# Kernel optimization log

Measured on AMD Instinct MI355X. Metric: run time of the kernel, lower is better.

Reference implementation:

```python
import jax, jax.numpy as jnp
import numpy as np

B, L, D, H, DH, FF = 4, 1024, 1024, 16, 64, 4096
EPS = 1e-5


def _layer_norm(x, g, b):
    m = jnp.mean(x, -1, keepdims=True)
    v = jnp.mean((x - m) ** 2, -1, keepdims=True)
    return (x - m) * jax.lax.rsqrt(v + EPS) * g + b


def setup_inputs() -> dict:
    key = jax.random.key(0)
    ks = jax.random.split(key, 20)
    s = 0.02  # param init scale
    return {
        "x": jax.random.normal(ks[0], (B, L, D), jnp.float32),
        "adj_mask_matrix": jax.random.uniform(ks[1], (B * H, L, L), jnp.float32),
        "com_mask_matrix": jax.random.uniform(ks[2], (B * H, L, L), jnp.float32),
        "lattice_rel": jax.random.normal(ks[3], (2, 1, 1, DH), jnp.float32),
        "Wq": jax.random.normal(ks[4], (D, D), jnp.float32) * s,
        "bq": jnp.zeros((D,), jnp.float32),
        "Wk": jax.random.normal(ks[5], (D, D), jnp.float32) * s,
        "bk": jnp.zeros((D,), jnp.float32),
        "Wv": jax.random.normal(ks[6], (D, D), jnp.float32) * s,
        "bv": jnp.zeros((D,), jnp.float32),
        "Wo": jax.random.normal(ks[7], (D, D), jnp.float32) * s,
        "bo": jnp.zeros((D,), jnp.float32),
        "ln1_scale": jnp.ones((D,), jnp.float32),
        "ln1_bias": jnp.zeros((D,), jnp.float32),
        "W1": jax.random.normal(ks[8], (D, FF), jnp.float32) * s,
        "b1": jnp.zeros((FF,), jnp.float32),
        "W2": jax.random.normal(ks[9], (FF, D), jnp.float32) * s,
        "b2": jnp.zeros((D,), jnp.float32),
        "ln2_scale": jnp.ones((D,), jnp.float32),
        "ln2_bias": jnp.zeros((D,), jnp.float32),
    }


def reference(x, adj_mask_matrix, com_mask_matrix, lattice_rel,
              Wq, bq, Wk, bk, Wv, bv, Wo, bo, ln1_scale, ln1_bias,
              W1, b1, W2, b2, ln2_scale, ln2_bias):
    Bsz, Ln, Dm = x.shape
    # QKV projections; flat reshape [B,L,H*dh] -> [B*H,L,dh] matches torch .view
    Q = (x @ Wq + bq).reshape(Bsz * H, Ln, DH)
    K = (x @ Wk + bk).reshape(Bsz * H, Ln, DH)
    V = (x @ Wv + bv).reshape(Bsz * H, Ln, DH)
    scale = DH ** (-0.5)
    adj_rel = lattice_rel[0]  # [1,1,dh] broadcasts over (B*H, L)
    com_rel = lattice_rel[1]
    att_adj = jnp.einsum('bqd,bkd->bqk', Q + adj_rel, K + adj_rel) * scale
    att_com = jnp.einsum('bqd,bkd->bqk', Q + com_rel, K + com_rel) * scale
    # post-softmax multiplicative masking, then sum of the two attention maps
    mask_att = (jax.nn.softmax(att_adj, axis=-1) * adj_mask_matrix
                + jax.nn.softmax(att_com, axis=-1) * com_mask_matrix)
    context = jnp.matmul(mask_att, V).reshape(Bsz, Ln, H * DH)
    out = _layer_norm(context @ Wo + bo + x, ln1_scale, ln1_bias)
    ff = jax.nn.relu(out @ W1 + b1) @ W2 + b2
    return _layer_norm(ff + out, ln2_scale, ln2_bias)
```

## Files before the change

kernel.cpp:

```cpp
#include <hip/hip_runtime.h>
#include <hip/hip_bf16.h>

typedef __attribute__((ext_vector_type(8))) short s16x8;
typedef __attribute__((ext_vector_type(4))) float f32x4;
typedef unsigned short u16;
typedef unsigned int u32;

__device__ __forceinline__ u16 f2b(float f) {
    u32 u = __float_as_uint(f);
    u32 r = (u + 0x7fffu + ((u >> 16) & 1u)) >> 16;
    return (u16)r;
}

#define MFMA16(a, b, c) __builtin_amdgcn_mfma_f32_16x16x32_bf16(a, b, c, 0, 0, 0)
#define GLDS(gp, lp)                                                              \
    __builtin_amdgcn_global_load_lds((const __attribute__((address_space(1))) void*)(gp), \
                                     (__attribute__((address_space(3))) void*)(lp), 16, 0, 0)
#define SB() __builtin_amdgcn_sched_barrier(0)

__global__ void k_f2b(const float* __restrict__ in, u16* __restrict__ out, int n4) {
    int i = blockIdx.x * 256 + threadIdx.x;
    if (i >= n4) return;
    float4 v = ((const float4*)in)[i];
    ushort4 o;
    o.x = f2b(v.x); o.y = f2b(v.y); o.z = f2b(v.z); o.w = f2b(v.w);
    ((ushort4*)out)[i] = o;
}

__global__ void k_wtrans(const float* __restrict__ W, u16* __restrict__ Wt, int K, int N) {
    __shared__ float t[32][33];
    int bx = blockIdx.x * 32, by = blockIdx.y * 32;
    int tx = threadIdx.x, ty = threadIdx.y;
    for (int i = 0; i < 32; i += 8)
        t[ty + i][tx] = W[(size_t)(by + ty + i) * N + bx + tx];
    __syncthreads();
    for (int i = 0; i < 32; i += 8)
        Wt[(size_t)(bx + ty + i) * K + by + tx] = f2b(t[tx][ty + i]);
}

__global__ __launch_bounds__(256) void gemm_qkv(const u16* __restrict__ A, const u16* __restrict__ Bt,
                                                const float* __restrict__ bq, const float* __restrict__ bk,
                                                const float* __restrict__ bv, const float* __restrict__ rel,
                                                u16* __restrict__ Qa, u16* __restrict__ Qc,
                                                u16* __restrict__ Ka, u16* __restrict__ Kc,
                                                u16* __restrict__ Vt) {
    __shared__ __align__(16) short lA[128 * 64];
    __shared__ __align__(16) short lB[128 * 64];
    const int tid = threadIdx.x, lane = tid & 63, w = tid >> 6;
    const int l15 = lane & 15, lg = lane >> 4;
    const int wr = w >> 1, wc = w & 1;
    const int m0 = blockIdx.y * 128, n0 = blockIdx.x * 128;
    const int KK = 1024;
    f32x4 acc[4][4] = {};

    for (int k0 = 0; k0 < KK; k0 += 64) {
        #pragma unroll
        for (int i = 0; i < 4; i++) {
            int chunk = w * 4 + i;
            int arow = m0 + chunk * 8 + (lane >> 3);
            GLDS(A + (size_t)arow * KK + k0 + (lane & 7) * 8, (short*)lA + chunk * 512);
            int brow = n0 + chunk * 8 + (lane >> 3);
            GLDS(Bt + (size_t)brow * KK + k0 + (lane & 7) * 8, (short*)lB + chunk * 512);
        }
        __syncthreads();
        #pragma unroll
        for (int ks = 0; ks < 2; ks++) {
            s16x8 af[4], bfr[4];
            #pragma unroll
            for (int m = 0; m < 4; m++)
                af[m] = *(const s16x8*)&lA[(wr * 64 + m * 16 + l15) * 64 + ks * 32 + lg * 8];
            #pragma unroll
            for (int n = 0; n < 4; n++)
                bfr[n] = *(const s16x8*)&lB[(wc * 64 + n * 16 + l15) * 64 + ks * 32 + lg * 8];
            #pragma unroll
            for (int m = 0; m < 4; m++)
                #pragma unroll
                for (int n = 0; n < 4; n++)
                    acc[m][n] = MFMA16(af[m], bfr[n], acc[m][n]);
        }
        __syncthreads();
    }
    const int rbase = m0 + wr * 64, cbase = n0 + wc * 64;
    const int seg = cbase >> 10;
    #pragma unroll
    for (int m = 0; m < 4; m++)
        #pragma unroll
        for (int n = 0; n < 4; n++) {
            int col = cbase + n * 16 + l15;
            int c1 = col & 1023, d = col & 63;
            int row0 = rbase + m * 16 + lg * 4;
            if (seg == 0) {
                float bb = bq[c1], r0 = rel[d], r1 = rel[64 + d];
                #pragma unroll
                for (int r = 0; r < 4; r++) {
                    float v = acc[m][n][r] + bb;
                    size_t o = (size_t)(row0 + r) * 1024 + c1;
                    Qa[o] = f2b(v + r0);
                    Qc[o] = f2b(v + r1);
                }
            } else if (seg == 1) {
                float bb = bk[c1], r0 = rel[d], r1 = rel[64 + d];
                #pragma unroll
                for (int r = 0; r < 4; r++) {
                    float v = acc[m][n][r] + bb;
                    size_t o = (size_t)(row0 + r) * 1024 + c1;
                    Ka[o] = f2b(v + r0);
                    Kc[o] = f2b(v + r1);
                }
            } else {
                float bb = bv[c1];
                #pragma unroll
                for (int r = 0; r < 4; r++) {
                    int row = row0 + r;
                    size_t o = (size_t)(row >> 6) * 65536 + (size_t)d * 1024 + (row & 63) * 16 + (c1 >> 6);
                    Vt[o] = f2b(acc[m][n][r] + bb);
                }
            }
        }
}

template <int EPI>
__global__ __launch_bounds__(256) void gemm_bt(const u16* __restrict__ A, const u16* __restrict__ Bt,
                                               void* __restrict__ Cv, int M, int N, int K,
                                               const float* __restrict__ bias) {
    __shared__ __align__(16) short lA[128 * 64];
    __shared__ __align__(16) short lB[128 * 64];
    const int tid = threadIdx.x, lane = tid & 63, w = tid >> 6;
    const int l15 = lane & 15, lg = lane >> 4;
    const int wr = w >> 1, wc = w & 1;
    const int m0 = blockIdx.y * 128, n0 = blockIdx.x * 128;
    f32x4 acc[4][4] = {};

    for (int k0 = 0; k0 < K; k0 += 64) {
        #pragma unroll
        for (int i = 0; i < 4; i++) {
            int chunk = w * 4 + i;
            int arow = m0 + chunk * 8 + (lane >> 3);
            GLDS(A + (size_t)arow * K + k0 + (lane & 7) * 8, (short*)lA + chunk * 512);
            int brow = n0 + chunk * 8 + (lane >> 3);
            GLDS(Bt + (size_t)brow * K + k0 + (lane & 7) * 8, (short*)lB + chunk * 512);
        }
        __syncthreads();
        #pragma unroll
        for (int ks = 0; ks < 2; ks++) {
            s16x8 af[4], bfr[4];
            #pragma unroll
            for (int m = 0; m < 4; m++)
                af[m] = *(const s16x8*)&lA[(wr * 64 + m * 16 + l15) * 64 + ks * 32 + lg * 8];
            #pragma unroll
            for (int n = 0; n < 4; n++)
                bfr[n] = *(const s16x8*)&lB[(wc * 64 + n * 16 + l15) * 64 + ks * 32 + lg * 8];
            #pragma unroll
            for (int m = 0; m < 4; m++)
                #pragma unroll
                for (int n = 0; n < 4; n++)
                    acc[m][n] = MFMA16(af[m], bfr[n], acc[m][n]);
        }
        __syncthreads();
    }
    const int rbase = m0 + wr * 64, cbase = n0 + wc * 64;
    #pragma unroll
    for (int m = 0; m < 4; m++)
        #pragma unroll
        for (int n = 0; n < 4; n++) {
            int col = cbase + n * 16 + l15;
            int row0 = rbase + m * 16 + lg * 4;
            u16* C = (u16*)Cv;
            float bv = bias[col];
            #pragma unroll
            for (int r = 0; r < 4; r++)
                C[(size_t)(row0 + r) * N + col] = f2b(fmaxf(acc[m][n][r] + bv, 0.f));
        }
}

__global__ __launch_bounds__(256) void gemm_bt64(const u16* __restrict__ A, const u16* __restrict__ Bt,
                                                 float* __restrict__ C, int M, int N, int K) {
    __shared__ __align__(16) short lA[128 * 64];
    __shared__ __align__(16) short lB[64 * 64];
    const int tid = threadIdx.x, lane = tid & 63, w = tid >> 6;
    const int l15 = lane & 15, lg = lane >> 4;
    const int m0 = blockIdx.y * 128, n0 = blockIdx.x * 64;
    f32x4 acc[2][4] = {};

    for (int k0 = 0; k0 < K; k0 += 64) {
        #pragma unroll
        for (int i = 0; i < 4; i++) {
            int chunk = w * 4 + i;
            int arow = m0 + chunk * 8 + (lane >> 3);
            GLDS(A + (size_t)arow * K + k0 + (lane & 7) * 8, (short*)lA + chunk * 512);
        }
        #pragma unroll
        for (int i = 0; i < 2; i++) {
            int chunk = w * 2 + i;
            int brow = n0 + chunk * 8 + (lane >> 3);
            GLDS(Bt + (size_t)brow * K + k0 + (lane & 7) * 8, (short*)lB + chunk * 512);
        }
        __syncthreads();
        #pragma unroll
        for (int ks = 0; ks < 2; ks++) {
            s16x8 af[2], bfr[4];
            #pragma unroll
            for (int m = 0; m < 2; m++)
                af[m] = *(const s16x8*)&lA[(w * 32 + m * 16 + l15) * 64 + ks * 32 + lg * 8];
            #pragma unroll
            for (int n = 0; n < 4; n++)
                bfr[n] = *(const s16x8*)&lB[(n * 16 + l15) * 64 + ks * 32 + lg * 8];
            #pragma unroll
            for (int m = 0; m < 2; m++)
                #pragma unroll
                for (int n = 0; n < 4; n++)
                    acc[m][n] = MFMA16(af[m], bfr[n], acc[m][n]);
        }
        __syncthreads();
    }
    #pragma unroll
    for (int m = 0; m < 2; m++)
        #pragma unroll
        for (int n = 0; n < 4; n++) {
            int col = n0 + n * 16 + l15;
            int row0 = m0 + w * 32 + m * 16 + lg * 4;
            #pragma unroll
            for (int r = 0; r < 4; r++)
                C[(size_t)(row0 + r) * N + col] = acc[m][n][r];
        }
}

__global__ __launch_bounds__(256) void k_attnf(const u16* __restrict__ Qa, const u16* __restrict__ Qc,
                                               const u16* __restrict__ Ka, const u16* __restrict__ Kc,
                                               const u16* __restrict__ Vt,
                                               const float* __restrict__ adjm, const float* __restrict__ comm,
                                               float* __restrict__ ctxA, float* __restrict__ ctxC) {
    const int bid = blockIdx.x;
    const int xcd = bid & 7, j = bid >> 3;
    const int g = xcd * 8 + (j & 7), qt = j >> 3;
    const int s = blockIdx.z;
    const u16* __restrict__ Q = s ? Qc : Qa;
    const u16* __restrict__ K = s ? Kc : Ka;
    const float* __restrict__ mask = s ? comm : adjm;
    float* __restrict__ ctxp = s ? ctxC : ctxA;

    const int tid = threadIdx.x, lane = tid & 63, w = tid >> 6;
    const int l15 = lane & 15, lg = lane >> 4;
    __shared__ __align__(16) float lE[4][16][68];

    const int q0 = qt * 64 + w * 16;
    const size_t gQ = (size_t)g * 65536;
    const float* __restrict__ mrow = mask + (size_t)g * 1048576 + (size_t)(q0 + l15) * 1024 + lg * 8;
    const float scale = 0.125f;

    s16x8 qf[2];
    #pragma unroll
    for (int ks = 0; ks < 2; ks++)
        qf[ks] = *(const s16x8*)(Q + gQ + (size_t)(q0 + l15) * 64 + ks * 32 + lg * 8);

    f32x4 ca[4] = {};
    float la[4] = {0.f, 0.f, 0.f, 0.f};

    #pragma unroll 1
    for (int it = 0; it < 16; it++) {
        const int kb = it * 64;
        s16x8 kf[8];
        #pragma unroll
        for (int ks = 0; ks < 2; ks++)
            #pragma unroll
            for (int n = 0; n < 4; n++)
                kf[ks * 4 + n] = *(const s16x8*)(K + gQ + (size_t)(kb + n * 16 + l15) * 64 + ks * 32 + lg * 8);
        SB();
        s16x8 vf[8];
        float4 mf[4];
        #pragma unroll
        for (int ks = 0; ks < 2; ks++)
            #pragma unroll
            for (int d = 0; d < 4; d++)
                vf[ks * 4 + d] = *(const s16x8*)(Vt + gQ + (size_t)(d * 16 + l15) * 1024 + kb + ks * 32 + lg * 8);
        #pragma unroll
        for (int ks = 0; ks < 2; ks++) {
            mf[ks * 2 + 0] = *(const float4*)(mrow + kb + ks * 32);
            mf[ks * 2 + 1] = *(const float4*)(mrow + kb + ks * 32 + 4);
        }
        SB();
        f32x4 sa[4] = {};
        #pragma unroll
        for (int ks = 0; ks < 2; ks++)
            #pragma unroll
            for (int n = 0; n < 4; n++)
                sa[n] = MFMA16(qf[ks], kf[ks * 4 + n], sa[n]);
        #pragma unroll
        for (int n = 0; n < 4; n++)
            #pragma unroll
            for (int r = 0; r < 4; r++) {
                float e = __expf(sa[n][r] * scale);
                la[r] += e;
                lE[w][lg * 4 + r][n * 16 + l15] = e;
            }
        #pragma unroll
        for (int ks = 0; ks < 2; ks++) {
            const float* ep = &lE[w][l15][ks * 32 + lg * 8];
            float4 e0 = *(const float4*)ep, e1 = *(const float4*)(ep + 4);
            union { s16x8 v; u16 u[8]; } pf;
            pf.u[0] = f2b(e0.x * mf[ks * 2].x); pf.u[1] = f2b(e0.y * mf[ks * 2].y);
            pf.u[2] = f2b(e0.z * mf[ks * 2].z); pf.u[3] = f2b(e0.w * mf[ks * 2].w);
            pf.u[4] = f2b(e1.x * mf[ks * 2 + 1].x); pf.u[5] = f2b(e1.y * mf[ks * 2 + 1].y);
            pf.u[6] = f2b(e1.z * mf[ks * 2 + 1].z); pf.u[7] = f2b(e1.w * mf[ks * 2 + 1].w);
            #pragma unroll
            for (int d = 0; d < 4; d++)
                ca[d] = MFMA16(pf.v, vf[ks * 4 + d], ca[d]);
        }
        SB();
    }
    #pragma unroll
    for (int r = 0; r < 4; r++)
        #pragma unroll
        for (int m = 8; m >= 1; m >>= 1)
            la[r] += __shfl_xor(la[r], m);
    #pragma unroll
    for (int r = 0; r < 4; r++) {
        float il = 1.f / la[r];
        int row = q0 + lg * 4 + r;
        #pragma unroll
        for (int d = 0; d < 4; d++)
            ctxp[gQ + (size_t)row * 64 + d * 16 + l15] = ca[d][r] * il;
    }
}

__global__ void k_comb(const float* __restrict__ A, const float* __restrict__ C,
                       u16* __restrict__ out, int n4) {
    int i = blockIdx.x * 256 + threadIdx.x;
    if (i >= n4) return;
    float4 a = ((const float4*)A)[i];
    float4 c = ((const float4*)C)[i];
    ushort4 o;
    o.x = f2b(a.x + c.x); o.y = f2b(a.y + c.y);
    o.z = f2b(a.z + c.z); o.w = f2b(a.w + c.w);
    ((ushort4*)out)[i] = o;
}

__global__ __launch_bounds__(256) void k_ln(const float* __restrict__ a, const float* __restrict__ bias,
                                            const float* __restrict__ resid, const float* __restrict__ gamma,
                                            const float* __restrict__ beta, float* __restrict__ out,
                                            u16* __restrict__ outb) {
    const int row = blockIdx.x, tid = threadIdx.x;
    const size_t base = (size_t)row * 1024 + tid * 4;
    float4 av = *(const float4*)(a + base);
    float4 rv = *(const float4*)(resid + base);
    float4 bv = *(const float4*)(bias + tid * 4);
    float t0 = av.x + rv.x + bv.x, t1 = av.y + rv.y + bv.y;
    float t2 = av.z + rv.z + bv.z, t3 = av.w + rv.w + bv.w;
    __shared__ float red[4];
    float s = t0 + t1 + t2 + t3;
    #pragma unroll
    for (int m = 32; m >= 1; m >>= 1) s += __shfl_xor(s, m);
    int w = tid >> 6;
    if ((tid & 63) == 0) red[w] = s;
    __syncthreads();
    float mean = (red[0] + red[1] + red[2] + red[3]) * (1.f / 1024.f);
    float d0 = t0 - mean, d1 = t1 - mean, d2 = t2 - mean, d3 = t3 - mean;
    float q = d0 * d0 + d1 * d1 + d2 * d2 + d3 * d3;
    __syncthreads();
    #pragma unroll
    for (int m = 32; m >= 1; m >>= 1) q += __shfl_xor(q, m);
    if ((tid & 63) == 0) red[w] = q;
    __syncthreads();
    float var = (red[0] + red[1] + red[2] + red[3]) * (1.f / 1024.f);
    float rs = rsqrtf(var + 1e-5f);
    float4 gv = *(const float4*)(gamma + tid * 4);
    float4 bev = *(const float4*)(beta + tid * 4);
    float o0 = d0 * rs * gv.x + bev.x, o1 = d1 * rs * gv.y + bev.y;
    float o2 = d2 * rs * gv.z + bev.z, o3 = d3 * rs * gv.w + bev.w;
    *(float4*)(out + base) = make_float4(o0, o1, o2, o3);
    if (outb) {
        ushort4 ob;
        ob.x = f2b(o0); ob.y = f2b(o1); ob.z = f2b(o2); ob.w = f2b(o3);
        *(ushort4*)(outb + base) = ob;
    }
}

extern "C" void kernel_launch(void* const* d_in, const int* in_sizes, int n_in,
                              void* d_out, int out_size, void* d_ws, size_t ws_size,
                              hipStream_t stream) {
    const float* x    = (const float*)d_in[0];
    const float* adjm = (const float*)d_in[1];
    const float* comm = (const float*)d_in[2];
    const float* rel  = (const float*)d_in[3];
    const float* Wq   = (const float*)d_in[4];
    const float* bq   = (const float*)d_in[5];
    const float* Wk   = (const float*)d_in[6];
    const float* bk   = (const float*)d_in[7];
    const float* Wv   = (const float*)d_in[8];
    const float* bv   = (const float*)d_in[9];
    const float* Wo   = (const float*)d_in[10];
    const float* bo   = (const float*)d_in[11];
    const float* g1   = (const float*)d_in[12];
    const float* be1  = (const float*)d_in[13];
    const float* W1   = (const float*)d_in[14];
    const float* b1   = (const float*)d_in[15];
    const float* W2   = (const float*)d_in[16];
    const float* b2   = (const float*)d_in[17];
    const float* g2   = (const float*)d_in[18];
    const float* be2  = (const float*)d_in[19];
    float* out = (float*)d_out;

    char* ws = (char*)d_ws;
    const size_t MB = 1048576;
    u16*   xb    = (u16*)(ws + 0 * MB);
    u16*   Wqkvt = (u16*)(ws + 8 * MB);
    u16*   Wot   = (u16*)(ws + 14 * MB);
    u16*   W1t   = (u16*)(ws + 16 * MB);
    u16*   W2t   = (u16*)(ws + 24 * MB);
    u16*   Qab   = (u16*)(ws + 32 * MB);
    u16*   Qcb   = (u16*)(ws + 40 * MB);
    u16*   Kab   = (u16*)(ws + 48 * MB);
    u16*   Kcb   = (u16*)(ws + 56 * MB);
    u16*   Vtb   = (u16*)(ws + 64 * MB);
    float* ctxA  = (float*)(ws + 72 * MB);
    float* ctxC  = (float*)(ws + 88 * MB);
    u16*   ctx   = (u16*)(ws + 104 * MB);
    float* ctxWo = (float*)(ws + 32 * MB);
    float* out1  = (float*)(ws + 48 * MB);
    u16*   out1b = (u16*)(ws + 64 * MB);
    u16*   rb    = (u16*)(ws + 72 * MB);
    float* ff2   = (float*)(ws + 0 * MB);

    dim3 tb(32, 8);
    k_f2b<<<4096, 256, 0, stream>>>(x, xb, 1048576);
    k_wtrans<<<dim3(32, 32), tb, 0, stream>>>(Wq, Wqkvt, 1024, 1024);
    k_wtrans<<<dim3(32, 32), tb, 0, stream>>>(Wk, Wqkvt + 1024 * 1024, 1024, 1024);
    k_wtrans<<<dim3(32, 32), tb, 0, stream>>>(Wv, Wqkvt + 2 * 1024 * 1024, 1024, 1024);
    k_wtrans<<<dim3(32, 32), tb, 0, stream>>>(Wo, Wot, 1024, 1024);
    k_wtrans<<<dim3(128, 32), tb, 0, stream>>>(W1, W1t, 1024, 4096);
    k_wtrans<<<dim3(32, 128), tb, 0, stream>>>(W2, W2t, 4096, 1024);
    gemm_qkv<<<dim3(24, 32), 256, 0, stream>>>(xb, Wqkvt, bq, bk, bv, rel,
                                               Qab, Qcb, Kab, Kcb, Vtb);
    k_attnf<<<dim3(1024, 1, 2), 256, 0, stream>>>(Qab, Qcb, Kab, Kcb, Vtb, adjm, comm, ctxA, ctxC);
    k_comb<<<4096, 256, 0, stream>>>(ctxA, ctxC, ctx, 1048576);
    gemm_bt64<<<dim3(16, 32), 256, 0, stream>>>(ctx, Wot, ctxWo, 4096, 1024, 1024);
    k_ln<<<4096, 256, 0, stream>>>(ctxWo, bo, x, g1, be1, out1, out1b);
    gemm_bt<1><<<dim3(32, 32), 256, 0, stream>>>(out1b, W1t, rb, 4096, 4096, 1024, b1);
    gemm_bt64<<<dim3(16, 32), 256, 0, stream>>>(rb, W2t, ff2, 4096, 1024, 4096);
    k_ln<<<4096, 256, 0, stream>>>(ff2, b2, out1, g2, be2, out, nullptr);
}
```

Measured before the change: 600.0 us.

## Split attention into QK-exp and masked PV kernels, merging both branches

Replaces the fused per-branch attention kernel and the separate combine kernel with two kernels. The first computes both adjacency and commonality QK^T exponentials together, writing unnormalized bf16 exp tiles and row denominators to workspace. The second reads those tiles with both masks and V, and emits the combined normalized context directly in bf16. This removes the fp32 per-branch context buffers and the combine pass and shares V loads across branches. In exchange it materializes two full L×L bf16 score matrices in global memory, adding several hundred MB of traffic. It also needs a much larger workspace.

```diff
diff --git a/kernel.cpp b/kernel.cpp
--- a/kernel.cpp
+++ b/kernel.cpp
@@ -11,12 +11,14 @@
     u32 r = (u + 0x7fffu + ((u >> 16) & 1u)) >> 16;
     return (u16)r;
 }
+__device__ __forceinline__ float b2f(u16 b) {
+    return __uint_as_float(((u32)b) << 16);
+}
 
 #define MFMA16(a, b, c) __builtin_amdgcn_mfma_f32_16x16x32_bf16(a, b, c, 0, 0, 0)
 #define GLDS(gp, lp)                                                              \
     __builtin_amdgcn_global_load_lds((const __attribute__((address_space(1))) void*)(gp), \
                                      (__attribute__((address_space(3))) void*)(lp), 16, 0, 0)
-#define SB() __builtin_amdgcn_sched_barrier(0)
 
 __global__ void k_f2b(const float* __restrict__ in, u16* __restrict__ out, int n4) {
     int i = blockIdx.x * 256 + threadIdx.x;
@@ -225,114 +227,169 @@
         }
 }
 
-__global__ __launch_bounds__(256) void k_attnf(const u16* __restrict__ Qa, const u16* __restrict__ Qc,
-                                               const u16* __restrict__ Ka, const u16* __restrict__ Kc,
-                                               const u16* __restrict__ Vt,
-                                               const float* __restrict__ adjm, const float* __restrict__ comm,
-                                               float* __restrict__ ctxA, float* __restrict__ ctxC) {
+__global__ __launch_bounds__(256) void k_qke2(const u16* __restrict__ Qa, const u16* __restrict__ Qc,
+                                              const u16* __restrict__ Ka, const u16* __restrict__ Kc,
+                                              u16* __restrict__ Ea, u16* __restrict__ Ec,
+                                              float* __restrict__ denA, float* __restrict__ denC) {
     const int bid = blockIdx.x;
     const int xcd = bid & 7, j = bid >> 3;
     const int g = xcd * 8 + (j & 7), qt = j >> 3;
-    const int s = blockIdx.z;
-    const u16* __restrict__ Q = s ? Qc : Qa;
-    const u16* __restrict__ K = s ? Kc : Ka;
-    const float* __restrict__ mask = s ? comm : adjm;
-    float* __restrict__ ctxp = s ? ctxC : ctxA;
-
     const int tid = threadIdx.x, lane = tid & 63, w = tid >> 6;
     const int l15 = lane & 15, lg = lane >> 4;
-    __shared__ __align__(16) float lE[4][16][68];
+    __shared__ __align__(16) float lE[2][4][16][68];
 
     const int q0 = qt * 64 + w * 16;
     const size_t gQ = (size_t)g * 65536;
-    const float* __restrict__ mrow = mask + (size_t)g * 1048576 + (size_t)(q0 + l15) * 1024 + lg * 8;
+    const size_t ebase = ((((size_t)g * 16 + qt) * 4 + w) * 16384) + (size_t)lane * 8;
     const float scale = 0.125f;
 
-    s16x8 qf[2];
-    #pragma unroll
-    for (int ks = 0; ks < 2; ks++)
-        qf[ks] = *(const s16x8*)(Q + gQ + (size_t)(q0 + l15) * 64 + ks * 32 + lg * 8);
-
-    f32x4 ca[4] = {};
-    float la[4] = {0.f, 0.f, 0.f, 0.f};
+    s16x8 qa[2], qc[2];
+    #pragma unroll
+    for (int ks = 0; ks < 2; ks++) {
+        size_t off = gQ + (size_t)(q0 + l15) * 64 + ks * 32 + lg * 8;
+        qa[ks] = *(const s16x8*)(Qa + off);
+        qc[ks] = *(const s16x8*)(Qc + off);
+    }
+
+    float la[4] = {0.f, 0.f, 0.f, 0.f}, lc[4] = {0.f, 0.f, 0.f, 0.f};
 
     #pragma unroll 1
     for (int it = 0; it < 16; it++) {
         const int kb = it * 64;
-        s16x8 kf[8];
+        f32x4 sa[4] = {}, sc[4] = {};
         #pragma unroll
         for (int ks = 0; ks < 2; ks++)
             #pragma unroll
-            for (int n = 0; n < 4; n++)
-                kf[ks * 4 + n] = *(const s16x8*)(K + gQ + (size_t)(kb + n * 16 + l15) * 64 + ks * 32 + lg * 8);
-        SB();
-        s16x8 vf[8];
-        float4 mf[4];
-        #pragma unroll
-        for (int ks = 0; ks < 2; ks++)
+            for (int n = 0; n < 4; n++) {
+                size_t koff = gQ + (size_t)(kb + n * 16 + l15) * 64 + ks * 32 + lg * 8;
+                s16x8 kfa = *(const s16x8*)(Ka + koff);
+                s16x8 kfc = *(const s16x8*)(Kc + koff);
+                sa[n] = MFMA16(qa[ks], kfa, sa[n]);
+                sc[n] = MFMA16(qc[ks], kfc, sc[n]);
+            }
+        #pragma unroll
+        for (int n = 0; n < 4; n++)
+            #pragma unroll
+            for (int r = 0; r < 4; r++) {
+                float ea = __expf(sa[n][r] * scale);
+                float ec = __expf(sc[n][r] * scale);
+                la[r] += ea;
+                lc[r] += ec;
+                lE[0][w][lg * 4 + r][n * 16 + l15] = ea;
+                lE[1][w][lg * 4 + r][n * 16 + l15] = ec;
+            }
+        #pragma unroll
+        for (int ks = 0; ks < 2; ks++) {
+            const float* ep = &lE[0][w][l15][ks * 32 + lg * 8];
+            float4 e0 = *(const float4*)ep, e1 = *(const float4*)(ep + 4);
+            uint4 st;
+            st.x = (u32)f2b(e0.x) | ((u32)f2b(e0.y) << 16);
+            st.y = (u32)f2b(e0.z) | ((u32)f2b(e0.w) << 16);
+            st.z = (u32)f2b(e1.x) | ((u32)f2b(e1.y) << 16);
+            st.w = (u32)f2b(e1.z) | ((u32)f2b(e1.w) << 16);
+            *(uint4*)(Ea + ebase + (size_t)it * 1024 + ks * 512) = st;
+            const float* fp = &lE[1][w][l15][ks * 32 + lg * 8];
+            float4 f0 = *(const float4*)fp, f1 = *(const float4*)(fp + 4);
+            uint4 st2;
+            st2.x = (u32)f2b(f0.x) | ((u32)f2b(f0.y) << 16);
+            st2.y = (u32)f2b(f0.z) | ((u32)f2b(f0.w) << 16);
+            st2.z = (u32)f2b(f1.x) | ((u32)f2b(f1.y) << 16);
+            st2.w = (u32)f2b(f1.z) | ((u32)f2b(f1.w) << 16);
+            *(uint4*)(Ec + ebase + (size_t)it * 1024 + ks * 512) = st2;
+        }
+    }
+    #pragma unroll
+    for (int r = 0; r < 4; r++)
+        #pragma unroll
+        for (int m = 8; m >= 1; m >>= 1) {
+            la[r] += __shfl_xor(la[r], m);
+            lc[r] += __shfl_xor(lc[r], m);
+        }
+    if (l15 == 0) {
+        #pragma unroll
+        for (int r = 0; r < 4; r++) {
+            denA[g * 1024 + q0 + lg * 4 + r] = la[r];
+            denC[g * 1024 + q0 + lg * 4 + r] = lc[r];
+        }
+    }
+}
+
+__global__ __launch_bounds__(256) void k_pv2(const u16* __restrict__ Ea, const u16* __restrict__ Ec,
+                                             const u16* __restrict__ Vt,
+                                             const float* __restrict__ adjm, const float* __restrict__ comm,
+                                             const float* __restrict__ denA, const float* __restrict__ denC,
+                                             u16* __restrict__ ctx) {
+    const int bid = blockIdx.x;
+    const int xcd = bid & 7, j = bid >> 3;
+    const int g = xcd * 8 + (j & 7), qt = j >> 3;
+    const int tid = threadIdx.x, lane = tid & 63, w = tid >> 6;
+    const int l15 = lane & 15, lg = lane >> 4;
+
+    const int q0 = qt * 64 + w * 16;
+    const size_t gQ = (size_t)g * 65536;
+    const size_t mroff = (size_t)g * 1048576 + (size_t)(q0 + l15) * 1024 + lg * 8;
+    const float* __restrict__ mrow_a = adjm + mroff;
+    const float* __restrict__ mrow_c = comm + mroff;
+    const size_t ebase = ((((size_t)g * 16 + qt) * 4 + w) * 16384) + (size_t)lane * 8;
+
+    f32x4 ca[4] = {}, cc[4] = {};
+
+    #pragma unroll 2
+    for (int it = 0; it < 16; it++) {
+        const int kb = it * 64;
+        s16x8 ea[2], ec[2], vf[8];
+        float4 ma[4], mc[4];
+        #pragma unroll
+        for (int ks = 0; ks < 2; ks++) {
+            ea[ks] = *(const s16x8*)(Ea + ebase + (size_t)it * 1024 + ks * 512);
+            ec[ks] = *(const s16x8*)(Ec + ebase + (size_t)it * 1024 + ks * 512);
+            ma[ks * 2 + 0] = *(const float4*)(mrow_a + kb + ks * 32);
+            ma[ks * 2 + 1] = *(const float4*)(mrow_a + kb + ks * 32 + 4);
+            mc[ks * 2 + 0] = *(const float4*)(mrow_c + kb + ks * 32);
+            mc[ks * 2 + 1] = *(const float4*)(mrow_c + kb + ks * 32 + 4);
             #pragma unroll
             for (int d = 0; d < 4; d++)
                 vf[ks * 4 + d] = *(const s16x8*)(Vt + gQ + (size_t)(d * 16 + l15) * 1024 + kb + ks * 32 + lg * 8);
+        }
         #pragma unroll
         for (int ks = 0; ks < 2; ks++) {
-            mf[ks * 2 + 0] = *(const float4*)(mrow + kb + ks * 32);
-            mf[ks * 2 + 1] = *(const float4*)(mrow + kb + ks * 32 + 4);
-        }
-        SB();
-        f32x4 sa[4] = {};
-        #pragma unroll
-        for (int ks = 0; ks < 2; ks++)
-            #pragma unroll
-            for (int n = 0; n < 4; n++)
-                sa[n] = MFMA16(qf[ks], kf[ks * 4 + n], sa[n]);
-        #pragma unroll
-        for (int n = 0; n < 4; n++)
-            #pragma unroll
-            for (int r = 0; r < 4; r++) {
-                float e = __expf(sa[n][r] * scale);
-                la[r] += e;
-                lE[w][lg * 4 + r][n * 16 + l15] = e;
+            union { s16x8 v; u16 u[8]; } pa, pc;
+            pa.u[0] = f2b(b2f((u16)ea[ks][0]) * ma[ks * 2].x);
+            pa.u[1] = f2b(b2f((u16)ea[ks][1]) * ma[ks * 2].y);
+            pa.u[2] = f2b(b2f((u16)ea[ks][2]) * ma[ks * 2].z);
+            pa.u[3] = f2b(b2f((u16)ea[ks][3]) * ma[ks * 2].w);
+            pa.u[4] = f2b(b2f((u16)ea[ks][4]) * ma[ks * 2 + 1].x);
+            pa.u[5] = f2b(b2f((u16)ea[ks][5]) * ma[ks * 2 + 1].y);
+            pa.u[6] = f2b(b2f((u16)ea[ks][6]) * ma[ks * 2 + 1].z);
+            pa.u[7] = f2b(b2f((u16)ea[ks][7]) * ma[ks * 2 + 1].w);
+            pc.u[0] = f2b(b2f((u16)ec[ks][0]) * mc[ks * 2].x);
+            pc.u[1] = f2b(b2f((u16)ec[ks][1]) * mc[ks * 2].y);
+            pc.u[2] = f2b(b2f((u16)ec[ks][2]) * mc[ks * 2].z);
+            pc.u[3] = f2b(b2f((u16)ec[ks][3]) * mc[ks * 2].w);
+            pc.u[4] = f2b(b2f((u16)ec[ks][4]) * mc[ks * 2 + 1].x);
+            pc.u[5] = f2b(b2f((u16)ec[ks][5]) * mc[ks * 2 + 1].y);
+            pc.u[6] = f2b(b2f((u16)ec[ks][6]) * mc[ks * 2 + 1].z);
+            pc.u[7] = f2b(b2f((u16)ec[ks][7]) * mc[ks * 2 + 1].w);
+            #pragma unroll
+            for (int d = 0; d < 4; d++) {
+                ca[d] = MFMA16(pa.v, vf[ks * 4 + d], ca[d]);
+                cc[d] = MFMA16(pc.v, vf[ks * 4 + d], cc[d]);
             }
-        #pragma unroll
-        for (int ks = 0; ks < 2; ks++) {
-            const float* ep = &lE[w][l15][ks * 32 + lg * 8];
-            float4 e0 = *(const float4*)ep, e1 = *(const float4*)(ep + 4);
-            union { s16x8 v; u16 u[8]; } pf;
-            pf.u[0] = f2b(e0.x * mf[ks * 2].x); pf.u[1] = f2b(e0.y * mf[ks * 2].y);
-            pf.u[2] = f2b(e0.z * mf[ks * 2].z); pf.u[3] = f2b(e0.w * mf[ks * 2].w);
-            pf.u[4] = f2b(e1.x * mf[ks * 2 + 1].x); pf.u[5] = f2b(e1.y * mf[ks * 2 + 1].y);
-            pf.u[6] = f2b(e1.z * mf[ks * 2 + 1].z); pf.u[7] = f2b(e1.w * mf[ks * 2 + 1].w);
-            #pragma unroll
-            for (int d = 0; d < 4; d++)
-                ca[d] = MFMA16(pf.v, vf[ks * 4 + d], ca[d]);
-        }
-        SB();
-    }
-    #pragma unroll
-    for (int r = 0; r < 4; r++)
-        #pragma unroll
-        for (int m = 8; m >= 1; m >>= 1)
-            la[r] += __shfl_xor(la[r], m);
+        }
+    }
+    float ila[4], ilc[4];
     #pragma unroll
     for (int r = 0; r < 4; r++) {
-        float il = 1.f / la[r];
+        ila[r] = 1.f / denA[g * 1024 + q0 + lg * 4 + r];
+        ilc[r] = 1.f / denC[g * 1024 + q0 + lg * 4 + r];
+    }
+    #pragma unroll
+    for (int r = 0; r < 4; r++) {
         int row = q0 + lg * 4 + r;
         #pragma unroll
         for (int d = 0; d < 4; d++)
-            ctxp[gQ + (size_t)row * 64 + d * 16 + l15] = ca[d][r] * il;
-    }
-}
-
-__global__ void k_comb(const float* __restrict__ A, const float* __restrict__ C,
-                       u16* __restrict__ out, int n4) {
-    int i = blockIdx.x * 256 + threadIdx.x;
-    if (i >= n4) return;
-    float4 a = ((const float4*)A)[i];
-    float4 c = ((const float4*)C)[i];
-    ushort4 o;
-    o.x = f2b(a.x + c.x); o.y = f2b(a.y + c.y);
-    o.z = f2b(a.z + c.z); o.w = f2b(a.w + c.w);
-    ((ushort4*)out)[i] = o;
+            ctx[gQ + (size_t)row * 64 + d * 16 + l15] = f2b(ca[d][r] * ila[r] + cc[d][r] * ilc[r]);
+    }
 }
 
 __global__ __launch_bounds__(256) void k_ln(const float* __restrict__ a, const float* __restrict__ bias,
@@ -412,9 +469,11 @@
     u16*   Kab   = (u16*)(ws + 48 * MB);
     u16*   Kcb   = (u16*)(ws + 56 * MB);
     u16*   Vtb   = (u16*)(ws + 64 * MB);
-    float* ctxA  = (float*)(ws + 72 * MB);
-    float* ctxC  = (float*)(ws + 88 * MB);
-    u16*   ctx   = (u16*)(ws + 104 * MB);
+    u16*   Eab   = (u16*)(ws + 72 * MB);
+    u16*   Ecb   = (u16*)(ws + 200 * MB);
+    float* denA  = (float*)(ws + 328 * MB);
+    float* denC  = (float*)(ws + 329 * MB);
+    u16*   ctx   = (u16*)(ws + 330 * MB);
     float* ctxWo = (float*)(ws + 32 * MB);
     float* out1  = (float*)(ws + 48 * MB);
     u16*   out1b = (u16*)(ws + 64 * MB);
@@ -431,8 +490,8 @@
     k_wtrans<<<dim3(32, 128), tb, 0, stream>>>(W2, W2t, 4096, 1024);
     gemm_qkv<<<dim3(24, 32), 256, 0, stream>>>(xb, Wqkvt, bq, bk, bv, rel,
                                                Qab, Qcb, Kab, Kcb, Vtb);
-    k_attnf<<<dim3(1024, 1, 2), 256, 0, stream>>>(Qab, Qcb, Kab, Kcb, Vtb, adjm, comm, ctxA, ctxC);
-    k_comb<<<4096, 256, 0, stream>>>(ctxA, ctxC, ctx, 1048576);
+    k_qke2<<<1024, 256, 0, stream>>>(Qab, Qcb, Kab, Kcb, Eab, Ecb, denA, denC);
+    k_pv2<<<1024, 256, 0, stream>>>(Eab, Ecb, Vtb, adjm, comm, denA, denC, ctx);
     gemm_bt64<<<dim3(16, 32), 256, 0, stream>>>(ctx, Wot, ctxWo, 4096, 1024, 1024);
     k_ln<<<4096, 256, 0, stream>>>(ctxWo, bo, x, g1, be1, out1, out1b);
     gemm_bt<1><<<dim3(32, 32), 256, 0, stream>>>(out1b, W1t, rb, 4096, 4096, 1024, b1);
```

Measured after the change: 671.1 us. 1.12x slower.

## Share one QK^T across both lattice softmaxes via per-key exponential factors

Applied to the files above, without the earlier changes.

Expands (Q+r)(K+r)^T and drops the per-query terms, which cancel inside softmax, so a single Q·K^T score matrix serves both the adjacency and the commonality attention. The per-key term r·K is folded in as precomputed exp factors (fa, fc) that scale the shared exponentials. This removes the duplicated Q/K buffers and half the score MFMAs and exponentials. In exchange, the fused attention kernel is split into four passes (k_fvec, k_qke0, k_pmul, gemm_pv) that write and re-read full bf16 L×L score and probability matrices, adding a lot of HBM traffic. It also adds extra bf16 rounding of the exponentials.

```diff
diff --git a/kernel.cpp b/kernel.cpp
--- a/kernel.cpp
+++ b/kernel.cpp
@@ -11,12 +11,14 @@
     u32 r = (u + 0x7fffu + ((u >> 16) & 1u)) >> 16;
     return (u16)r;
 }
+__device__ __forceinline__ float b2f(u16 b) {
+    return __uint_as_float(((u32)b) << 16);
+}
 
 #define MFMA16(a, b, c) __builtin_amdgcn_mfma_f32_16x16x32_bf16(a, b, c, 0, 0, 0)
 #define GLDS(gp, lp)                                                              \
     __builtin_amdgcn_global_load_lds((const __attribute__((address_space(1))) void*)(gp), \
                                      (__attribute__((address_space(3))) void*)(lp), 16, 0, 0)
-#define SB() __builtin_amdgcn_sched_barrier(0)
 
 __global__ void k_f2b(const float* __restrict__ in, u16* __restrict__ out, int n4) {
     int i = blockIdx.x * 256 + threadIdx.x;
@@ -40,9 +42,8 @@
 
 __global__ __launch_bounds__(256) void gemm_qkv(const u16* __restrict__ A, const u16* __restrict__ Bt,
                                                 const float* __restrict__ bq, const float* __restrict__ bk,
-                                                const float* __restrict__ bv, const float* __restrict__ rel,
-                                                u16* __restrict__ Qa, u16* __restrict__ Qc,
-                                                u16* __restrict__ Ka, u16* __restrict__ Kc,
+                                                const float* __restrict__ bv,
+                                                u16* __restrict__ Qb, u16* __restrict__ Kb,
                                                 u16* __restrict__ Vt) {
     __shared__ __align__(16) short lA[128 * 64];
     __shared__ __align__(16) short lB[128 * 64];
@@ -90,23 +91,15 @@
             int c1 = col & 1023, d = col & 63;
             int row0 = rbase + m * 16 + lg * 4;
             if (seg == 0) {
-                float bb = bq[c1], r0 = rel[d], r1 = rel[64 + d];
-                #pragma unroll
-                for (int r = 0; r < 4; r++) {
-                    float v = acc[m][n][r] + bb;
-                    size_t o = (size_t)(row0 + r) * 1024 + c1;
-                    Qa[o] = f2b(v + r0);
-                    Qc[o] = f2b(v + r1);
-                }
+                float bb = bq[c1];
+                #pragma unroll
+                for (int r = 0; r < 4; r++)
+                    Qb[(size_t)(row0 + r) * 1024 + c1] = f2b(acc[m][n][r] + bb);
             } else if (seg == 1) {
-                float bb = bk[c1], r0 = rel[d], r1 = rel[64 + d];
-                #pragma unroll
-                for (int r = 0; r < 4; r++) {
-                    float v = acc[m][n][r] + bb;
-                    size_t o = (size_t)(row0 + r) * 1024 + c1;
-                    Ka[o] = f2b(v + r0);
-                    Kc[o] = f2b(v + r1);
-                }
+                float bb = bk[c1];
+                #pragma unroll
+                for (int r = 0; r < 4; r++)
+                    Kb[(size_t)(row0 + r) * 1024 + c1] = f2b(acc[m][n][r] + bb);
             } else {
                 float bb = bv[c1];
                 #pragma unroll
@@ -225,114 +218,193 @@
         }
 }
 
-__global__ __launch_bounds__(256) void k_attnf(const u16* __restrict__ Qa, const u16* __restrict__ Qc,
-                                               const u16* __restrict__ Ka, const u16* __restrict__ Kc,
-                                               const u16* __restrict__ Vt,
-                                               const float* __restrict__ adjm, const float* __restrict__ comm,
-                                               float* __restrict__ ctxA, float* __restrict__ ctxC) {
+__global__ void k_fvec(const u16* __restrict__ Kb, const float* __restrict__ rel,
+                       float* __restrict__ fa, float* __restrict__ fc) {
+    __shared__ float rs[128];
+    const int g = blockIdx.x, tid = threadIdx.x;
+    if (tid < 128) rs[tid] = rel[tid];
+    __syncthreads();
+    for (int k = tid; k < 1024; k += 256) {
+        const u16* kr = Kb + (size_t)g * 65536 + (size_t)k * 64;
+        float sa = 0.f, sc = 0.f;
+        #pragma unroll
+        for (int j = 0; j < 8; j++) {
+            s16x8 v = *(const s16x8*)(kr + j * 8);
+            #pragma unroll
+            for (int e = 0; e < 8; e++) {
+                float kv = b2f((u16)v[e]);
+                sa += kv * rs[j * 8 + e];
+                sc += kv * rs[64 + j * 8 + e];
+            }
+        }
+        fa[g * 1024 + k] = __expf(sa * 0.125f);
+        fc[g * 1024 + k] = __expf(sc * 0.125f);
+    }
+}
+
+__global__ __launch_bounds__(256, 2) void k_qke0(const u16* __restrict__ Qb, const u16* __restrict__ Kb,
+                                                 const float* __restrict__ fa, const float* __restrict__ fc,
+                                                 u16* __restrict__ E0,
+                                                 float* __restrict__ la_, float* __restrict__ lc_) {
     const int bid = blockIdx.x;
     const int xcd = bid & 7, j = bid >> 3;
     const int g = xcd * 8 + (j & 7), qt = j >> 3;
-    const int s = blockIdx.z;
-    const u16* __restrict__ Q = s ? Qc : Qa;
-    const u16* __restrict__ K = s ? Kc : Ka;
-    const float* __restrict__ mask = s ? comm : adjm;
-    float* __restrict__ ctxp = s ? ctxC : ctxA;
-
     const int tid = threadIdx.x, lane = tid & 63, w = tid >> 6;
     const int l15 = lane & 15, lg = lane >> 4;
     __shared__ __align__(16) float lE[4][16][68];
 
     const int q0 = qt * 64 + w * 16;
     const size_t gQ = (size_t)g * 65536;
-    const float* __restrict__ mrow = mask + (size_t)g * 1048576 + (size_t)(q0 + l15) * 1024 + lg * 8;
     const float scale = 0.125f;
 
     s16x8 qf[2];
     #pragma unroll
     for (int ks = 0; ks < 2; ks++)
-        qf[ks] = *(const s16x8*)(Q + gQ + (size_t)(q0 + l15) * 64 + ks * 32 + lg * 8);
-
-    f32x4 ca[4] = {};
-    float la[4] = {0.f, 0.f, 0.f, 0.f};
+        qf[ks] = *(const s16x8*)(Qb + gQ + (size_t)(q0 + l15) * 64 + ks * 32 + lg * 8);
+
+    float la[4] = {0.f, 0.f, 0.f, 0.f}, lc[4] = {0.f, 0.f, 0.f, 0.f};
+    const int srow = lane >> 2, sjj = lane & 3;
 
     #pragma unroll 1
     for (int it = 0; it < 16; it++) {
         const int kb = it * 64;
+        f32x4 sa[4] = {};
         s16x8 kf[8];
         #pragma unroll
         for (int ks = 0; ks < 2; ks++)
             #pragma unroll
             for (int n = 0; n < 4; n++)
-                kf[ks * 4 + n] = *(const s16x8*)(K + gQ + (size_t)(kb + n * 16 + l15) * 64 + ks * 32 + lg * 8);
-        SB();
-        s16x8 vf[8];
-        float4 mf[4];
-        #pragma unroll
-        for (int ks = 0; ks < 2; ks++)
-            #pragma unroll
-            for (int d = 0; d < 4; d++)
-                vf[ks * 4 + d] = *(const s16x8*)(Vt + gQ + (size_t)(d * 16 + l15) * 1024 + kb + ks * 32 + lg * 8);
-        #pragma unroll
-        for (int ks = 0; ks < 2; ks++) {
-            mf[ks * 2 + 0] = *(const float4*)(mrow + kb + ks * 32);
-            mf[ks * 2 + 1] = *(const float4*)(mrow + kb + ks * 32 + 4);
-        }
-        SB();
-        f32x4 sa[4] = {};
+                kf[ks * 4 + n] = *(const s16x8*)(Kb + gQ + (size_t)(kb + n * 16 + l15) * 64 + ks * 32 + lg * 8);
         #pragma unroll
         for (int ks = 0; ks < 2; ks++)
             #pragma unroll
             for (int n = 0; n < 4; n++)
                 sa[n] = MFMA16(qf[ks], kf[ks * 4 + n], sa[n]);
         #pragma unroll
-        for (int n = 0; n < 4; n++)
+        for (int n = 0; n < 4; n++) {
+            float fav = fa[g * 1024 + kb + n * 16 + l15];
+            float fcv = fc[g * 1024 + kb + n * 16 + l15];
             #pragma unroll
             for (int r = 0; r < 4; r++) {
-                float e = __expf(sa[n][r] * scale);
-                la[r] += e;
-                lE[w][lg * 4 + r][n * 16 + l15] = e;
+                float er = b2f(f2b(__expf(sa[n][r] * scale)));
+                la[r] += er * fav;
+                lc[r] += er * fcv;
+                lE[w][lg * 4 + r][n * 16 + l15] = er;
             }
+        }
+        {
+            const float* lp = &lE[w][srow][sjj * 16];
+            uint4 p0, p1;
+            p0.x = (u32)f2b(lp[0]) | ((u32)f2b(lp[1]) << 16);
+            p0.y = (u32)f2b(lp[2]) | ((u32)f2b(lp[3]) << 16);
+            p0.z = (u32)f2b(lp[4]) | ((u32)f2b(lp[5]) << 16);
+            p0.w = (u32)f2b(lp[6]) | ((u32)f2b(lp[7]) << 16);
+            p1.x = (u32)f2b(lp[8]) | ((u32)f2b(lp[9]) << 16);
+            p1.y = (u32)f2b(lp[10]) | ((u32)f2b(lp[11]) << 16);
+            p1.z = (u32)f2b(lp[12]) | ((u32)f2b(lp[13]) << 16);
+            p1.w = (u32)f2b(lp[14]) | ((u32)f2b(lp[15]) << 16);
+            u16* ep = E0 + (size_t)g * 1048576 + (size_t)(q0 + srow) * 1024 + kb + sjj * 16;
+            *(uint4*)ep = p0;
+            *(uint4*)(ep + 8) = p1;
+        }
+    }
+    #pragma unroll
+    for (int r = 0; r < 4; r++)
+        #pragma unroll
+        for (int m = 8; m >= 1; m >>= 1) {
+            la[r] += __shfl_xor(la[r], m);
+            lc[r] += __shfl_xor(lc[r], m);
+        }
+    if (l15 == 0) {
+        #pragma unroll
+        for (int r = 0; r < 4; r++) {
+            la_[g * 1024 + q0 + lg * 4 + r] = la[r];
+            lc_[g * 1024 + q0 + lg * 4 + r] = lc[r];
+        }
+    }
+}
+
+__global__ void k_pmul(const u16* __restrict__ E0, const float* __restrict__ Ma, const float* __restrict__ Mc,
+                       const float* __restrict__ fa, const float* __restrict__ fc,
+                       const float* __restrict__ la, const float* __restrict__ lc,
+                       u16* __restrict__ P) {
+    int idx = blockIdx.x * 256 + threadIdx.x;
+    int g = idx >> 17;
+    int q = (idx >> 7) & 1023;
+    int k0 = (idx & 127) * 8;
+    size_t base = (size_t)idx * 8;
+    s16x8 e = *(const s16x8*)(E0 + base);
+    float4 m0 = *(const float4*)(Ma + base), m1 = *(const float4*)(Ma + base + 4);
+    float4 n0 = *(const float4*)(Mc + base), n1 = *(const float4*)(Mc + base + 4);
+    int fi = g * 1024 + k0;
+    float4 a0 = *(const float4*)(fa + fi), a1 = *(const float4*)(fa + fi + 4);
+    float4 c0 = *(const float4*)(fc + fi), c1 = *(const float4*)(fc + fi + 4);
+    float ila = 1.f / la[g * 1024 + q];
+    float ilc = 1.f / lc[g * 1024 + q];
+    uint4 o;
+    o.x = (u32)f2b(b2f((u16)e[0]) * (a0.x * m0.x * ila + c0.x * n0.x * ilc)) |
+          ((u32)f2b(b2f((u16)e[1]) * (a0.y * m0.y * ila + c0.y * n0.y * ilc)) << 16);
+    o.y = (u32)f2b(b2f((u16)e[2]) * (a0.z * m0.z * ila + c0.z * n0.z * ilc)) |
+          ((u32)f2b(b2f((u16)e[3]) * (a0.w * m0.w * ila + c0.w * n0.w * ilc)) << 16);
+    o.z = (u32)f2b(b2f((u16)e[4]) * (a1.x * m1.x * ila + c1.x * n1.x * ilc)) |
+          ((u32)f2b(b2f((u16)e[5]) * (a1.y * m1.y * ila + c1.y * n1.y * ilc)) << 16);
+    o.w = (u32)f2b(b2f((u16)e[6]) * (a1.z * m1.z * ila + c1.z * n1.z * ilc)) |
+          ((u32)f2b(b2f((u16)e[7]) * (a1.w * m1.w * ila + c1.w * n1.w * ilc)) << 16);
+    *(uint4*)(P + base) = o;
+}
+
+__global__ __launch_bounds__(256) void gemm_pv(const u16* __restrict__ P, const u16* __restrict__ Vt,
+                                               u16* __restrict__ ctx) {
+    __shared__ __align__(16) short lA[128 * 64];
+    __shared__ __align__(16) short lB[64 * 64];
+    const int tid = threadIdx.x, lane = tid & 63, w = tid >> 6;
+    const int l15 = lane & 15, lg = lane >> 4;
+    const int g = blockIdx.y, m0 = blockIdx.x * 128;
+    const u16* A = P + (size_t)g * 1048576;
+    const u16* Bt = Vt + (size_t)g * 65536;
+    f32x4 acc[2][4] = {};
+
+    for (int k0 = 0; k0 < 1024; k0 += 64) {
+        #pragma unroll
+        for (int i = 0; i < 4; i++) {
+            int chunk = w * 4 + i;
+            int arow = m0 + chunk * 8 + (lane >> 3);
+            GLDS(A + (size_t)arow * 1024 + k0 + (lane & 7) * 8, (short*)lA + chunk * 512);
+        }
+        #pragma unroll
+        for (int i = 0; i < 2; i++) {
+            int chunk = w * 2 + i;
+            int brow = chunk * 8 + (lane >> 3);
+            GLDS(Bt + (size_t)brow * 1024 + k0 + (lane & 7) * 8, (short*)lB + chunk * 512);
+        }
+        __syncthreads();
         #pragma unroll
         for (int ks = 0; ks < 2; ks++) {
-            const float* ep = &lE[w][l15][ks * 32 + lg * 8];
-            float4 e0 = *(const float4*)ep, e1 = *(const float4*)(ep + 4);
-            union { s16x8 v; u16 u[8]; } pf;
-            pf.u[0] = f2b(e0.x * mf[ks * 2].x); pf.u[1] = f2b(e0.y * mf[ks * 2].y);
-            pf.u[2] = f2b(e0.z * mf[ks * 2].z); pf.u[3] = f2b(e0.w * mf[ks * 2].w);
-            pf.u[4] = f2b(e1.x * mf[ks * 2 + 1].x); pf.u[5] = f2b(e1.y * mf[ks * 2 + 1].y);
-            pf.u[6] = f2b(e1.z * mf[ks * 2 + 1].z); pf.u[7] = f2b(e1.w * mf[ks * 2 + 1].w);
-            #pragma unroll
-            for (int d = 0; d < 4; d++)
-                ca[d] = MFMA16(pf.v, vf[ks * 4 + d], ca[d]);
-        }
-        SB();
-    }
-    #pragma unroll
-    for (int r = 0; r < 4; r++)
-        #pragma unroll
-        for (int m = 8; m >= 1; m >>= 1)
-            la[r] += __shfl_xor(la[r], m);
-    #pragma unroll
-    for (int r = 0; r < 4; r++) {
-        float il = 1.f / la[r];
-        int row = q0 + lg * 4 + r;
-        #pragma unroll
-        for (int d = 0; d < 4; d++)
-            ctxp[gQ + (size_t)row * 64 + d * 16 + l15] = ca[d][r] * il;
-    }
-}
-
-__global__ void k_comb(const float* __restrict__ A, const float* __restrict__ C,
-                       u16* __restrict__ out, int n4) {
-    int i = blockIdx.x * 256 + threadIdx.x;
-    if (i >= n4) return;
-    float4 a = ((const float4*)A)[i];
-    float4 c = ((const float4*)C)[i];
-    ushort4 o;
-    o.x = f2b(a.x + c.x); o.y = f2b(a.y + c.y);
-    o.z = f2b(a.z + c.z); o.w = f2b(a.w + c.w);
-    ((ushort4*)out)[i] = o;
+            s16x8 af[2], bfr[4];
+            #pragma unroll
+            for (int m = 0; m < 2; m++)
+                af[m] = *(const s16x8*)&lA[(w * 32 + m * 16 + l15) * 64 + ks * 32 + lg * 8];
+            #pragma unroll
+            for (int n = 0; n < 4; n++)
+                bfr[n] = *(const s16x8*)&lB[(n * 16 + l15) * 64 + ks * 32 + lg * 8];
+            #pragma unroll
+            for (int m = 0; m < 2; m++)
+                #pragma unroll
+                for (int n = 0; n < 4; n++)
+                    acc[m][n] = MFMA16(af[m], bfr[n], acc[m][n]);
+        }
+        __syncthreads();
+    }
+    #pragma unroll
+    for (int m = 0; m < 2; m++)
+        #pragma unroll
+        for (int n = 0; n < 4; n++) {
+            int col = n * 16 + l15;
+            int row0 = m0 + w * 32 + m * 16 + lg * 4;
+            #pragma unroll
+            for (int r = 0; r < 4; r++)
+                ctx[(size_t)g * 65536 + (size_t)(row0 + r) * 64 + col] = f2b(acc[m][n][r]);
+        }
 }
 
 __global__ __launch_bounds__(256) void k_ln(const float* __restrict__ a, const float* __restrict__ bias,
@@ -407,19 +479,21 @@
     u16*   Wot   = (u16*)(ws + 14 * MB);
     u16*   W1t   = (u16*)(ws + 16 * MB);
     u16*   W2t   = (u16*)(ws + 24 * MB);
-    u16*   Qab   = (u16*)(ws + 32 * MB);
-    u16*   Qcb   = (u16*)(ws + 40 * MB);
-    u16*   Kab   = (u16*)(ws + 48 * MB);
-    u16*   Kcb   = (u16*)(ws + 56 * MB);
-    u16*   Vtb   = (u16*)(ws + 64 * MB);
-    float* ctxA  = (float*)(ws + 72 * MB);
-    float* ctxC  = (float*)(ws + 88 * MB);
-    u16*   ctx   = (u16*)(ws + 104 * MB);
-    float* ctxWo = (float*)(ws + 32 * MB);
-    float* out1  = (float*)(ws + 48 * MB);
-    u16*   out1b = (u16*)(ws + 64 * MB);
-    u16*   rb    = (u16*)(ws + 72 * MB);
-    float* ff2   = (float*)(ws + 0 * MB);
+    u16*   Qb    = (u16*)(ws + 32 * MB);
+    u16*   Kb    = (u16*)(ws + 40 * MB);
+    u16*   Vtb   = (u16*)(ws + 48 * MB);
+    float* faB   = (float*)(ws + 56 * MB);
+    float* fcB   = (float*)(ws + 56 * MB + 262144);
+    float* laB   = (float*)(ws + 56 * MB + 524288);
+    float* lcB   = (float*)(ws + 56 * MB + 786432);
+    u16*   E0b   = (u16*)(ws + 57 * MB);
+    u16*   Pb    = (u16*)(ws + 185 * MB);
+    u16*   ctx   = (u16*)(ws + 313 * MB);
+    float* ctxWo = (float*)(ws + 57 * MB);
+    float* out1  = (float*)(ws + 73 * MB);
+    u16*   out1b = (u16*)(ws + 89 * MB);
+    u16*   rb    = (u16*)(ws + 97 * MB);
+    float* ff2   = (float*)(ws + 129 * MB);
 
     dim3 tb(32, 8);
     k_f2b<<<4096, 256, 0, stream>>>(x, xb, 1048576);
@@ -429,10 +503,11 @@
     k_wtrans<<<dim3(32, 32), tb, 0, stream>>>(Wo, Wot, 1024, 1024);
     k_wtrans<<<dim3(128, 32), tb, 0, stream>>>(W1, W1t, 1024, 4096);
     k_wtrans<<<dim3(32, 128), tb, 0, stream>>>(W2, W2t, 4096, 1024);
-    gemm_qkv<<<dim3(24, 32), 256, 0, stream>>>(xb, Wqkvt, bq, bk, bv, rel,
-                                               Qab, Qcb, Kab, Kcb, Vtb);
-    k_attnf<<<dim3(1024, 1, 2), 256, 0, stream>>>(Qab, Qcb, Kab, Kcb, Vtb, adjm, comm, ctxA, ctxC);
-    k_comb<<<4096, 256, 0, stream>>>(ctxA, ctxC, ctx, 1048576);
+    gemm_qkv<<<dim3(24, 32), 256, 0, stream>>>(xb, Wqkvt, bq, bk, bv, Qb, Kb, Vtb);
+    k_fvec<<<64, 256, 0, stream>>>(Kb, rel, faB, fcB);
+    k_qke0<<<1024, 256, 0, stream>>>(Qb, Kb, faB, fcB, E0b, laB, lcB);
+    k_pmul<<<32768, 256, 0, stream>>>(E0b, adjm, comm, faB, fcB, laB, lcB, Pb);
+    gemm_pv<<<dim3(8, 64), 256, 0, stream>>>(Pb, Vtb, ctx);
     gemm_bt64<<<dim3(16, 32), 256, 0, stream>>>(ctx, Wot, ctxWo, 4096, 1024, 1024);
     k_ln<<<4096, 256, 0, stream>>>(ctxWo, bo, x, g1, be1, out1, out1b);
     gemm_bt<1><<<dim3(32, 32), 256, 0, stream>>>(out1b, W1t, rb, 4096, 4096, 1024, b1);
```

Result: faster. 562.5 us (-6.3%).
